# Optimization experiments

Measured on AMD Instinct MI355X. Metric: run time of the kernel, lower is better.

Reference implementation:

```python
import jax, jax.numpy as jnp
import numpy as np

GRID = 5
ELEMS = GRID * GRID  # 25 values per puzzle grid


def _dup_count(rows):
    """rows: [B, 5, 5]; counts, per row, elements equal to an earlier element
    in the same row (i.e. 5 - num_unique per row, summed). Returns scalar."""
    # eq[b, i, j, k] = rows[b, i, j] == rows[b, i, k]
    eq = rows[:, :, :, None] == rows[:, :, None, :]
    # strictly-lower mask over (j, k): only k < j counts as 'seen earlier'
    earlier = jnp.tril(jnp.ones((GRID, GRID), dtype=bool), k=-1)
    dup = jnp.any(eq & earlier, axis=-1)  # [B, 5, 5]
    return jnp.sum(dup.astype(jnp.float32))


def setup_inputs() -> dict:
    key = jax.random.key(0)
    k1, k2 = jax.random.split(key)
    n = 26214400  # 1,048,576 grids * 25
    preds = jax.random.normal(k1, (n,), dtype=jnp.float32)
    targets = jax.random.randint(k2, (n,), 0, 6, dtype=jnp.int32)
    return {"preds": preds, "targets": targets}


def reference(preds, targets):
    preds_flat = preds.reshape(-1)
    # loss1: mean absolute error against float-cast integer targets
    loss1 = jnp.mean(jnp.abs(preds_flat - targets.astype(jnp.float32)))

    batch_size = targets.shape[0] // ELEMS
    # duplicate counting runs on detached predictions (original uses .detach().cpu().numpy())
    grids = jax.lax.stop_gradient(preds_flat).reshape(batch_size, GRID, GRID)
    total_dup = _dup_count(grids) + _dup_count(jnp.swapaxes(grids, 1, 2))
    loss2 = total_dup / batch_size * 0.1

    # out-of-bounds penalty: .any().item() has no gradient path
    p = jax.lax.stop_gradient(preds_flat)
    oob = jnp.any((p < 0.5) | (p > 5.5))
    return loss1 + loss2 + jnp.where(oob, jnp.float32(1000.0), jnp.float32(0.0))
```

## Files before the change

### kernel.cpp

```cpp
#include <hip/hip_runtime.h>


#define BLOCK 256
#define WAVES_PER_BLOCK 4
#define TILE 1600
#define NBLOCKS 512
#define NWAVES WAVES_PER_BLOCK

#define GLOBAL_AS(p) ((__attribute__((address_space(1))) void*)(p))
#define LDS_AS(p)    ((__attribute__((address_space(3))) void*)(p))

__device__ __forceinline__ int grid_dups_reg(const float* p) {
    int ldup = 0;
    #pragma unroll
    for (int r = 0; r < 5; ++r) {
        const float a = p[r*5+0], b = p[r*5+1], c = p[r*5+2],
                    d = p[r*5+3], e = p[r*5+4];
        ldup += (int)(b == a);
        ldup += (int)((c == a) | (c == b));
        ldup += (int)((d == a) | (d == b) | (d == c));
        ldup += (int)((e == a) | (e == b) | (e == c) | (e == d));
    }
    #pragma unroll
    for (int q = 0; q < 5; ++q) {
        const float a = p[q+0], b = p[q+5], c = p[q+10],
                    d = p[q+15], e = p[q+20];
        ldup += (int)(b == a);
        ldup += (int)((c == a) | (c == b));
        ldup += (int)((d == a) | (d == b) | (d == c));
        ldup += (int)((e == a) | (e == b) | (e == c) | (e == d));
    }
    return ldup;
}

__global__ __launch_bounds__(BLOCK) void puzzle_main(
    const float* __restrict__ preds, const int* __restrict__ tgts,
    long long n_total,
    float* __restrict__ blk_sum, int* __restrict__ blk_dup,
    int* __restrict__ blk_oob)
{
    __shared__ float lds_p[WAVES_PER_BLOCK * TILE];
    __shared__ int   lds_t[WAVES_PER_BLOCK * TILE];
    __shared__ float s_sum[NWAVES];
    __shared__ int   s_dup[NWAVES];
    __shared__ int   s_oob[NWAVES];

    const int tid  = threadIdx.x;
    const int lane = tid & 63;
    const int wv   = tid >> 6;

    const long long total_tiles = n_total / TILE;
    const int total_waves = gridDim.x * WAVES_PER_BLOCK;
    const int gwave = blockIdx.x * WAVES_PER_BLOCK + wv;

    float* __restrict__ wp = &lds_p[wv * TILE];
    int*   __restrict__ wt = &lds_t[wv * TILE];

    float lsum = 0.0f;
    int   ldup = 0;
    float mn =  1e30f;
    float mx = -1e30f;

    for (long long t = gwave; t < total_tiles; t += total_waves) {
        const float* srcp = preds + t * TILE;
        const int*   srct = tgts  + t * TILE;

        __builtin_amdgcn_sched_barrier(0);
        #pragma unroll
        for (int c = 0; c < 6; ++c)
            __builtin_amdgcn_global_load_lds(GLOBAL_AS(srcp + c*256 + lane*4),
                                             LDS_AS(wp + c*256), 16, 0, 0);
        __builtin_amdgcn_global_load_lds(GLOBAL_AS(srcp + 1536 + lane),
                                         LDS_AS(wp + 1536), 4, 0, 0);
        #pragma unroll
        for (int c = 0; c < 6; ++c)
            __builtin_amdgcn_global_load_lds(GLOBAL_AS(srct + c*256 + lane*4),
                                             LDS_AS(wt + c*256), 16, 0, 0);
        __builtin_amdgcn_global_load_lds(GLOBAL_AS(srct + 1536 + lane),
                                         LDS_AS(wt + 1536), 4, 0, 0);

        __builtin_amdgcn_s_waitcnt(0x0F70);
        __builtin_amdgcn_sched_barrier(0);

        const float* __restrict__ g  = wp + lane * 25;
        const int*   __restrict__ ti = wt + lane * 25;

        float p[25];
        #pragma unroll
        for (int j = 0; j < 25; ++j) p[j] = g[j];

        #pragma unroll
        for (int j = 0; j < 25; ++j) {
            lsum += fabsf(p[j] - (float)ti[j]);
            mn = fminf(mn, p[j]);
            mx = fmaxf(mx, p[j]);
        }
        ldup += grid_dups_reg(p);
    }

    const long long rem = n_total - total_tiles * TILE;
    if (rem > 0 && gwave == total_waves - 1) {
        const int ngrids = (int)(rem / 25);
        if (lane < ngrids) {
            const float* srcp = preds + total_tiles * TILE + (long long)lane * 25;
            const int*   srct = tgts  + total_tiles * TILE + (long long)lane * 25;
            float p[25];
            #pragma unroll
            for (int j = 0; j < 25; ++j) p[j] = srcp[j];
            #pragma unroll
            for (int j = 0; j < 25; ++j) {
                lsum += fabsf(p[j] - (float)srct[j]);
                mn = fminf(mn, p[j]);
                mx = fmaxf(mx, p[j]);
            }
            ldup += grid_dups_reg(p);
        }
    }

    #pragma unroll
    for (int off = 32; off > 0; off >>= 1) {
        lsum += __shfl_down(lsum, off, 64);
        ldup += __shfl_down(ldup, off, 64);
        mn = fminf(mn, __shfl_down(mn, off, 64));
        mx = fmaxf(mx, __shfl_down(mx, off, 64));
    }
    if (lane == 0) {
        s_sum[wv] = lsum;
        s_dup[wv] = ldup;
        s_oob[wv] = (int)((mn < 0.5f) | (mx > 5.5f));
    }
    __syncthreads();
    if (tid == 0) {
        float bs = 0.0f; int bd = 0, bo = 0;
        #pragma unroll
        for (int w = 0; w < NWAVES; ++w) { bs += s_sum[w]; bd += s_dup[w]; bo |= s_oob[w]; }
        blk_sum[blockIdx.x] = bs;
        blk_dup[blockIdx.x] = bd;
        blk_oob[blockIdx.x] = bo;
    }
}

#define FBLOCK 256
#define FNWAVES (FBLOCK / 64)

__global__ __launch_bounds__(FBLOCK) void puzzle_final(
    const float* __restrict__ blk_sum, const int* __restrict__ blk_dup,
    const int* __restrict__ blk_oob, int nblocks,
    long long n_total, long long batch, float* __restrict__ out)
{
    __shared__ double s_sum[FNWAVES];
    __shared__ int    s_dup[FNWAVES];
    __shared__ int    s_oob[FNWAVES];

    double lsum = 0.0;
    int ldup = 0, loob = 0;
    for (int i = threadIdx.x; i < nblocks; i += FBLOCK) {
        lsum += (double)blk_sum[i];
        ldup += blk_dup[i];
        loob |= blk_oob[i];
    }
    #pragma unroll
    for (int off = 32; off > 0; off >>= 1) {
        lsum += __shfl_down(lsum, off, 64);
        ldup += __shfl_down(ldup, off, 64);
        loob |= __shfl_down(loob, off, 64);
    }
    const int wave = threadIdx.x >> 6;
    if ((threadIdx.x & 63) == 0) { s_sum[wave] = lsum; s_dup[wave] = ldup; s_oob[wave] = loob; }
    __syncthreads();
    if (threadIdx.x == 0) {
        double bs = 0.0; int bd = 0, bo = 0;
        #pragma unroll
        for (int w = 0; w < FNWAVES; ++w) { bs += s_sum[w]; bd += s_dup[w]; bo |= s_oob[w]; }
        const float loss1 = (float)(bs / (double)n_total);
        const float loss2 = (float)((double)bd * 0.1 / (double)batch);
        out[0] = loss1 + loss2 + (bo ? 1000.0f : 0.0f);
    }
}

extern "C" void kernel_launch(void* const* d_in, const int* in_sizes, int n_in,
                              void* d_out, int out_size, void* d_ws, size_t ws_size,
                              hipStream_t stream) {
    const float* preds = (const float*)d_in[0];
    const int*   tgts  = (const int*)d_in[1];
    float* out = (float*)d_out;

    const long long n = (long long)in_sizes[0];
    const long long batch = n / 25;

    float* blk_sum = (float*)d_ws;
    int*   blk_dup = (int*)(blk_sum + NBLOCKS);
    int*   blk_oob = (int*)(blk_dup + NBLOCKS);

    puzzle_main<<<NBLOCKS, BLOCK, 0, stream>>>(preds, tgts, n,
                                               blk_sum, blk_dup, blk_oob);
    puzzle_final<<<1, FBLOCK, 0, stream>>>(blk_sum, blk_dup, blk_oob,
                                           NBLOCKS, n, batch, out);
}
```

Baseline: 221.9 us.

## Replace async global-to-LDS loads with register float4 loads and LDS only for preds

Preds and targets are now loaded into registers with coalesced float4/int4 global loads instead of going through async global_load_lds. The MAE and min/max terms are computed directly from those registers. Only preds are staged in LDS so each lane can read its own 25-element grid for the duplicate check. Dropping the targets buffer halves LDS use per block, and the grid grows from 512 to 1536 blocks to raise occupancy and memory parallelism. The trade-off is more VGPR pressure, and LDS writes and reads within a wave with no explicit barrier, relying on the wave executing in lockstep.

New measurement: 223.2 us. Within noise of the previous version (+0.6%).

```diff
diff --git a/kernel.cpp b/kernel.cpp
--- a/kernel.cpp
+++ b/kernel.cpp
@@ -2,15 +2,11 @@
 
 
 #define BLOCK 256
-#define WAVES_PER_BLOCK 4
+#define WPB 4
 #define TILE 1600
-#define NBLOCKS 512
-#define NWAVES WAVES_PER_BLOCK
+#define NBLOCKS 1536
 
-#define GLOBAL_AS(p) ((__attribute__((address_space(1))) void*)(p))
-#define LDS_AS(p)    ((__attribute__((address_space(3))) void*)(p))
-
-__device__ __forceinline__ int grid_dups_reg(const float* p) {
+__device__ __forceinline__ int grid_dups(const float* __restrict__ p) {
     int ldup = 0;
     #pragma unroll
     for (int r = 0; r < 5; ++r) {
@@ -39,22 +35,21 @@
     float* __restrict__ blk_sum, int* __restrict__ blk_dup,
     int* __restrict__ blk_oob)
 {
-    __shared__ float lds_p[WAVES_PER_BLOCK * TILE];
-    __shared__ int   lds_t[WAVES_PER_BLOCK * TILE];
-    __shared__ float s_sum[NWAVES];
-    __shared__ int   s_dup[NWAVES];
-    __shared__ int   s_oob[NWAVES];
+    __shared__ float lds_p[WPB * TILE];
+    __shared__ float s_sum[WPB];
+    __shared__ int   s_dup[WPB];
+    __shared__ int   s_oob[WPB];
 
     const int tid  = threadIdx.x;
     const int lane = tid & 63;
     const int wv   = tid >> 6;
 
     const long long total_tiles = n_total / TILE;
-    const int total_waves = gridDim.x * WAVES_PER_BLOCK;
-    const int gwave = blockIdx.x * WAVES_PER_BLOCK + wv;
+    const int total_waves = gridDim.x * WPB;
+    const int gwave = blockIdx.x * WPB + wv;
 
     float* __restrict__ wp = &lds_p[wv * TILE];
-    int*   __restrict__ wt = &lds_t[wv * TILE];
+    float4* __restrict__ wp4 = reinterpret_cast<float4*>(wp);
 
     float lsum = 0.0f;
     int   ldup = 0;
@@ -62,58 +57,52 @@
     float mx = -1e30f;
 
     for (long long t = gwave; t < total_tiles; t += total_waves) {
-        const float* srcp = preds + t * TILE;
-        const int*   srct = tgts  + t * TILE;
+        const float4* __restrict__ p4 = (const float4*)(preds + t * TILE);
+        const int4*   __restrict__ t4 = (const int4*)(tgts  + t * TILE);
 
-        __builtin_amdgcn_sched_barrier(0);
+        float4 p[6];
+        int4   ti[6];
         #pragma unroll
-        for (int c = 0; c < 6; ++c)
-            __builtin_amdgcn_global_load_lds(GLOBAL_AS(srcp + c*256 + lane*4),
-                                             LDS_AS(wp + c*256), 16, 0, 0);
-        __builtin_amdgcn_global_load_lds(GLOBAL_AS(srcp + 1536 + lane),
-                                         LDS_AS(wp + 1536), 4, 0, 0);
+        for (int k = 0; k < 6; ++k) p[k]  = p4[lane + 64 * k];
         #pragma unroll
-        for (int c = 0; c < 6; ++c)
-            __builtin_amdgcn_global_load_lds(GLOBAL_AS(srct + c*256 + lane*4),
-                                             LDS_AS(wt + c*256), 16, 0, 0);
-        __builtin_amdgcn_global_load_lds(GLOBAL_AS(srct + 1536 + lane),
-                                         LDS_AS(wt + 1536), 4, 0, 0);
-
-        __builtin_amdgcn_s_waitcnt(0x0F70);
-        __builtin_amdgcn_sched_barrier(0);
-
-        const float* __restrict__ g  = wp + lane * 25;
-        const int*   __restrict__ ti = wt + lane * 25;
-
-        float p[25];
-        #pragma unroll
-        for (int j = 0; j < 25; ++j) p[j] = g[j];
+        for (int k = 0; k < 6; ++k) ti[k] = t4[lane + 64 * k];
+        const float ptl = preds[t * TILE + 1536 + lane];
+        const int   ttl = tgts [t * TILE + 1536 + lane];
 
         #pragma unroll
-        for (int j = 0; j < 25; ++j) {
-            lsum += fabsf(p[j] - (float)ti[j]);
-            mn = fminf(mn, p[j]);
-            mx = fmaxf(mx, p[j]);
+        for (int k = 0; k < 6; ++k) {
+            wp4[lane + 64 * k] = p[k];
+            lsum += fabsf(p[k].x - (float)ti[k].x);
+            lsum += fabsf(p[k].y - (float)ti[k].y);
+            lsum += fabsf(p[k].z - (float)ti[k].z);
+            lsum += fabsf(p[k].w - (float)ti[k].w);
+            mn = fminf(mn, fminf(fminf(p[k].x, p[k].y), fminf(p[k].z, p[k].w)));
+            mx = fmaxf(mx, fmaxf(fmaxf(p[k].x, p[k].y), fmaxf(p[k].z, p[k].w)));
         }
-        ldup += grid_dups_reg(p);
+        wp[1536 + lane] = ptl;
+        lsum += fabsf(ptl - (float)ttl);
+        mn = fminf(mn, ptl);
+        mx = fmaxf(mx, ptl);
+
+        ldup += grid_dups(wp + lane * 25);
     }
 
     const long long rem = n_total - total_tiles * TILE;
     if (rem > 0 && gwave == total_waves - 1) {
         const int ngrids = (int)(rem / 25);
         if (lane < ngrids) {
-            const float* srcp = preds + total_tiles * TILE + (long long)lane * 25;
-            const int*   srct = tgts  + total_tiles * TILE + (long long)lane * 25;
-            float p[25];
+            const float* sp = preds + total_tiles * TILE + (long long)lane * 25;
+            const int*   st = tgts  + total_tiles * TILE + (long long)lane * 25;
+            float q[25];
             #pragma unroll
-            for (int j = 0; j < 25; ++j) p[j] = srcp[j];
+            for (int j = 0; j < 25; ++j) q[j] = sp[j];
             #pragma unroll
             for (int j = 0; j < 25; ++j) {
-                lsum += fabsf(p[j] - (float)srct[j]);
-                mn = fminf(mn, p[j]);
-                mx = fmaxf(mx, p[j]);
+                lsum += fabsf(q[j] - (float)st[j]);
+                mn = fminf(mn, q[j]);
+                mx = fmaxf(mx, q[j]);
             }
-            ldup += grid_dups_reg(p);
+            ldup += grid_dups(q);
         }
     }
 
@@ -133,7 +122,7 @@
     if (tid == 0) {
         float bs = 0.0f; int bd = 0, bo = 0;
         #pragma unroll
-        for (int w = 0; w < NWAVES; ++w) { bs += s_sum[w]; bd += s_dup[w]; bo |= s_oob[w]; }
+        for (int w = 0; w < WPB; ++w) { bs += s_sum[w]; bd += s_dup[w]; bo |= s_oob[w]; }
         blk_sum[blockIdx.x] = bs;
         blk_dup[blockIdx.x] = bd;
         blk_oob[blockIdx.x] = bo;
```
